# Optimization experiments

Measured on AMD Instinct MI355X. Metric: run time of the kernel, lower is better.

## Reference

```python
import jax, jax.numpy as jnp
import numpy as np

B, H, S, D = 2, 16, 2048, 128  # batch, heads, seq_len, head_dim (hidden=2048, heads=16)


def setup_inputs() -> dict:
    key = jax.random.key(0)
    kq, kk, kv = jax.random.split(key, 3)
    q = jax.random.normal(kq, (B, H, S, D), dtype=jnp.float32)
    k = jax.random.normal(kk, (B, H, S, D), dtype=jnp.float32)
    v = jax.random.normal(kv, (B, H, S, D), dtype=jnp.float32)
    return {"q": q, "k": k, "v": v}


def reference(q, k, v):
    # scores = (q @ k^T) / sqrt(head_dim)  -> [B, H, S, S]
    scaling = 1.0 / jnp.sqrt(jnp.asarray(q.shape[-1], dtype=q.dtype))
    scores = jnp.einsum('bhqd,bhkd->bhqk', q, k) * scaling
    # softmax over keys (dropout p=0.0 -> identity in eval / p=0)
    weights = jax.nn.softmax(scores, axis=-1)
    # out = weights @ v -> [B, H, S, D]
    return jnp.einsum('bhqk,bhkd->bhqd', weights, v)
```

## Files before the change

kernel.cpp:

```cpp
#include <hip/hip_runtime.h>
#include <stdint.h>

typedef __attribute__((ext_vector_type(4))) float f32x4;
typedef __attribute__((ext_vector_type(16))) float f32x16;
typedef __attribute__((ext_vector_type(8))) short bf16x8;

constexpr int S_ = 2048;
constexpr int D_ = 128;
constexpr int BH = 32;
constexpr int KB = 64;
constexpr int NT = S_ / KB;
constexpr float QSCALE = 0.08838834764831845f * 1.4426950408889634f;

__device__ __forceinline__ short f2bf(float f) {
  uint32_t u = __float_as_uint(f);
  u += 0x7fffu + ((u >> 16) & 1u);
  return (short)(u >> 16);
}

__device__ __forceinline__ void gll16(const void* g, void* l) {
  __builtin_amdgcn_global_load_lds(
      (const __attribute__((address_space(1))) void*)g,
      (__attribute__((address_space(3))) void*)l, 16, 0, 0);
}

__global__ void prep_k(const float* __restrict__ k, short* __restrict__ kb) {
  const size_t N8 = (size_t)BH * S_ * D_ / 8;
  size_t i = (size_t)blockIdx.x * blockDim.x + threadIdx.x;
  const size_t stride = (size_t)gridDim.x * blockDim.x;
  for (; i < N8; i += stride) {
    float4 a = reinterpret_cast<const float4*>(k)[i * 2];
    float4 b = reinterpret_cast<const float4*>(k)[i * 2 + 1];
    bf16x8 o;
    o[0] = f2bf(a.x); o[1] = f2bf(a.y); o[2] = f2bf(a.z); o[3] = f2bf(a.w);
    o[4] = f2bf(b.x); o[5] = f2bf(b.y); o[6] = f2bf(b.z); o[7] = f2bf(b.w);
    reinterpret_cast<bf16x8*>(kb)[i] = o;
  }
}

__global__ void prep_vt(const float* __restrict__ v, short* __restrict__ vt) {
  __shared__ __align__(16) short Lt[64][136];
  const int bh = blockIdx.x >> 5;
  const int s0 = (blockIdx.x & 31) * 64;
  const int t = threadIdx.x;
#pragma unroll
  for (int i = 0; i < 4; ++i) {
    int g = t + 256 * i;
    int r = g >> 4, c8 = g & 15;
    const float* src = v + ((size_t)bh * S_ + s0 + r) * D_ + c8 * 8;
    float4 f0 = *reinterpret_cast<const float4*>(src);
    float4 f1 = *reinterpret_cast<const float4*>(src + 4);
    bf16x8 o;
    o[0] = f2bf(f0.x); o[1] = f2bf(f0.y); o[2] = f2bf(f0.z); o[3] = f2bf(f0.w);
    o[4] = f2bf(f1.x); o[5] = f2bf(f1.y); o[6] = f2bf(f1.z); o[7] = f2bf(f1.w);
    *reinterpret_cast<bf16x8*>(&Lt[r][c8 * 8]) = o;
  }
  __syncthreads();
#pragma unroll
  for (int i = 0; i < 4; ++i) {
    int g = t * 4 + i;
    int d = g >> 3, s8 = g & 7;
    bf16x8 o;
#pragma unroll
    for (int j = 0; j < 8; ++j) o[j] = Lt[s8 * 8 + j][d];
    *reinterpret_cast<bf16x8*>(&vt[((size_t)bh * D_ + d) * S_ + s0 + s8 * 8]) = o;
  }
}

__global__ __launch_bounds__(256, 2) void attn_fwd_v4(
    const float* __restrict__ q, const short* __restrict__ kbf,
    const short* __restrict__ vt, float* __restrict__ out)
{
  __shared__ __align__(16) short Klds[2][64 * 128];
  __shared__ __align__(16) short Vlds[2][128 * 64];

  const int lid = blockIdx.x;
  const int swz = (lid & 7) * 64 + (lid >> 3);
  const int qt = swz & 15;
  const int bh = swz >> 4;

  const int tid = threadIdx.x;
  const int wid = tid >> 6;
  const int lane = tid & 63;
  const int l32 = lane & 31;
  const int hi = lane >> 5;

  const int qrow = qt * 128 + wid * 32 + l32;

  bf16x8 bq[8];
  {
    const float* qg = q + ((size_t)bh * S_ + qrow) * D_ + hi * 8;
#pragma unroll
    for (int s = 0; s < 8; ++s) {
      float4 f0 = *reinterpret_cast<const float4*>(qg + s * 16);
      float4 f1 = *reinterpret_cast<const float4*>(qg + s * 16 + 4);
      bf16x8 a;
      a[0] = f2bf(f0.x * QSCALE); a[1] = f2bf(f0.y * QSCALE);
      a[2] = f2bf(f0.z * QSCALE); a[3] = f2bf(f0.w * QSCALE);
      a[4] = f2bf(f1.x * QSCALE); a[5] = f2bf(f1.y * QSCALE);
      a[6] = f2bf(f1.z * QSCALE); a[7] = f2bf(f1.w * QSCALE);
      bq[s] = a;
    }
  }

  const short* kg = kbf + (size_t)bh * S_ * D_;
  const short* vg = vt + (size_t)bh * D_ * S_;

  auto stage = [&](int buf, int kv0) {
#pragma unroll
    for (int j = 0; j < 4; ++j)
      gll16(kg + (size_t)kv0 * D_ + lane * D_ + (j * 4 + wid) * 8,
            &Klds[buf][(j * 256 + wid * 64) * 8]);
#pragma unroll
    for (int j = 0; j < 4; ++j)
      gll16(vg + kv0 + (size_t)((wid & 1) * 64 + lane) * S_ + (j * 2 + (wid >> 1)) * 8,
            &Vlds[buf][(j * 256 + wid * 64) * 8]);
  };

  float m = -1e30f, l = 0.f;
  f32x16 oacc[4];
#pragma unroll
  for (int d0 = 0; d0 < 4; ++d0)
#pragma unroll
    for (int r = 0; r < 16; ++r) oacc[d0][r] = 0.f;

  stage(0, 0);
  int cur = 0;
  for (int t = 0; t < NT; ++t) {
    __syncthreads();
    if (t + 1 < NT) stage(cur ^ 1, (t + 1) * KB);

    const short* Kb = &Klds[cur][0];
    const short* Vb = &Vlds[cur][0];

    f32x16 sf0, sf1;
#pragma unroll
    for (int r = 0; r < 16; ++r) { sf0[r] = 0.f; sf1[r] = 0.f; }
    __builtin_amdgcn_s_setprio(1);
#pragma unroll
    for (int s = 0; s < 8; ++s) {
      bf16x8 k0 = *reinterpret_cast<const bf16x8*>(
          &Kb[((s * 2 + hi) * 64 + l32) * 8]);
      bf16x8 k1 = *reinterpret_cast<const bf16x8*>(
          &Kb[((s * 2 + hi) * 64 + 32 + l32) * 8]);
      sf0 = __builtin_amdgcn_mfma_f32_32x32x16_bf16(k0, bq[s], sf0, 0, 0, 0);
      sf1 = __builtin_amdgcn_mfma_f32_32x32x16_bf16(k1, bq[s], sf1, 0, 0, 0);
    }
    __builtin_amdgcn_s_setprio(0);

    float pm = fmaxf(sf0[0], sf0[1]);
#pragma unroll
    for (int r = 2; r < 16; ++r) pm = fmaxf(pm, sf0[r]);
#pragma unroll
    for (int r = 0; r < 16; ++r) pm = fmaxf(pm, sf1[r]);
    pm = fmaxf(pm, __shfl_xor(pm, 32, 64));
    if (__any(pm > m + 8.f)) {
      const float mo = m;
      m = fmaxf(mo, pm);
      const float al = exp2f(mo - m);
      l *= al;
#pragma unroll
      for (int d0 = 0; d0 < 4; ++d0)
#pragma unroll
        for (int r = 0; r < 16; ++r) oacc[d0][r] *= al;
    }

    float ps = 0.f;
#define PROCESS_CHUNK(SF, C)                                                    \
    {                                                                           \
      uint32_t w[8];                                                            \
      _Pragma("unroll")                                                         \
      for (int i2 = 0; i2 < 8; ++i2) {                                          \
        float e0 = exp2f(SF[2 * i2] - m);                                       \
        float e1 = exp2f(SF[2 * i2 + 1] - m);                                   \
        ps += e0 + e1;                                                          \
        asm("v_cvt_pk_bf16_f32 %0, %1, %2" : "=v"(w[i2]) : "v"(e0), "v"(e1));   \
      }                                                                         \
      asm("v_permlane32_swap_b32 %0, %1" : "+v"(w[0]), "+v"(w[2]));             \
      asm("v_permlane32_swap_b32 %0, %1" : "+v"(w[1]), "+v"(w[3]));             \
      asm("v_permlane32_swap_b32 %0, %1" : "+v"(w[4]), "+v"(w[6]));             \
      asm("v_permlane32_swap_b32 %0, %1" : "+v"(w[5]), "+v"(w[7]));             \
      union { int4 i4; bf16x8 b; } u0, u1;                                      \
      u0.i4 = (int4){(int)w[0], (int)w[1], (int)w[2], (int)w[3]};               \
      u1.i4 = (int4){(int)w[4], (int)w[5], (int)w[6], (int)w[7]};               \
      __builtin_amdgcn_s_setprio(1);                                            \
      _Pragma("unroll")                                                         \
      for (int d0 = 0; d0 < 4; ++d0) {                                          \
        bf16x8 av = *reinterpret_cast<const bf16x8*>(                           \
            &Vb[(((C) * 4 + hi) * 128 + d0 * 32 + l32) * 8]);                   \
        oacc[d0] = __builtin_amdgcn_mfma_f32_32x32x16_bf16(av, u0.b, oacc[d0], 0, 0, 0); \
      }                                                                         \
      _Pragma("unroll")                                                         \
      for (int d0 = 0; d0 < 4; ++d0) {                                          \
        bf16x8 av = *reinterpret_cast<const bf16x8*>(                           \
            &Vb[(((C) * 4 + 2 + hi) * 128 + d0 * 32 + l32) * 8]);               \
        oacc[d0] = __builtin_amdgcn_mfma_f32_32x32x16_bf16(av, u1.b, oacc[d0], 0, 0, 0); \
      }                                                                         \
      __builtin_amdgcn_s_setprio(0);                                            \
    }

    PROCESS_CHUNK(sf0, 0)
    PROCESS_CHUNK(sf1, 1)
#undef PROCESS_CHUNK

    ps += __shfl_xor(ps, 32, 64);
    l += ps;
    cur ^= 1;
  }

  const float inv = 1.0f / l;
  float* ob = out + ((size_t)bh * S_ + qrow) * D_;
#pragma unroll
  for (int d0 = 0; d0 < 4; ++d0)
#pragma unroll
    for (int r2 = 0; r2 < 4; ++r2) {
      float4 o4 = {oacc[d0][r2 * 4 + 0] * inv, oacc[d0][r2 * 4 + 1] * inv,
                   oacc[d0][r2 * 4 + 2] * inv, oacc[d0][r2 * 4 + 3] * inv};
      *reinterpret_cast<float4*>(ob + d0 * 32 + r2 * 8 + hi * 4) = o4;
    }
}

__global__ __launch_bounds__(256, 4) void attn_fwd_v1(
    const float* __restrict__ q, const float* __restrict__ k,
    const float* __restrict__ v, float* __restrict__ out)
{
  __shared__ __align__(16) short Klds[32 * 128];
  __shared__ __align__(16) short Vlds[128 * 40];
  __shared__ __align__(16) short Plds[4][16 * 40];
  const int lid = blockIdx.x;
  const int swz = (lid & 7) * 128 + (lid >> 3);
  const int qt = swz & 31;
  const int bh = swz >> 5;
  const int tid = threadIdx.x;
  const int wid = tid >> 6;
  const int lane = tid & 63;
  const int l16 = lane & 15;
  const int lhi = lane >> 4;
  const int qrow0 = qt * 64 + wid * 16;
  const float* qg = q + ((size_t)bh * S_ + qrow0 + l16) * D_;
  const float* kg = k + (size_t)bh * S_ * D_;
  const float* vg = v + (size_t)bh * S_ * D_;
  bf16x8 aq[4];
#pragma unroll
  for (int ks = 0; ks < 4; ++ks) {
    const float* p = qg + ks * 32 + lhi * 8;
    float4 f0 = *reinterpret_cast<const float4*>(p);
    float4 f1 = *reinterpret_cast<const float4*>(p + 4);
    bf16x8 a;
    a[0] = f2bf(f0.x * QSCALE); a[1] = f2bf(f0.y * QSCALE);
    a[2] = f2bf(f0.z * QSCALE); a[3] = f2bf(f0.w * QSCALE);
    a[4] = f2bf(f1.x * QSCALE); a[5] = f2bf(f1.y * QSCALE);
    a[6] = f2bf(f1.z * QSCALE); a[7] = f2bf(f1.w * QSCALE);
    aq[ks] = a;
  }
  float mrow[4], lrow[4];
  f32x4 oacc[8];
#pragma unroll
  for (int r = 0; r < 4; ++r) { mrow[r] = -1e30f; lrow[r] = 0.f; }
#pragma unroll
  for (int i = 0; i < 8; ++i) oacc[i] = (f32x4){0.f, 0.f, 0.f, 0.f};
  for (int t = 0; t < S_ / 32; ++t) {
    const int kv0 = t * 32;
    __syncthreads();
#pragma unroll
    for (int i = 0; i < 2; ++i) {
      const int g = tid * 2 + i;
      const int row = g >> 4;
      const int c8 = g & 15;
      const float* ksrc = kg + (size_t)(kv0 + row) * D_ + c8 * 8;
      float4 f0 = *reinterpret_cast<const float4*>(ksrc);
      float4 f1 = *reinterpret_cast<const float4*>(ksrc + 4);
      bf16x8 kk;
      kk[0] = f2bf(f0.x); kk[1] = f2bf(f0.y); kk[2] = f2bf(f0.z); kk[3] = f2bf(f0.w);
      kk[4] = f2bf(f1.x); kk[5] = f2bf(f1.y); kk[6] = f2bf(f1.z); kk[7] = f2bf(f1.w);
      *reinterpret_cast<bf16x8*>(
          &Klds[row * D_ + ((c8 * 8) ^ ((row & 7) << 3))]) = kk;
      const float* vsrc = vg + (size_t)(kv0 + row) * D_ + c8 * 8;
      float4 g0 = *reinterpret_cast<const float4*>(vsrc);
      float4 g1 = *reinterpret_cast<const float4*>(vsrc + 4);
      const int dbase = c8 * 8;
      Vlds[(dbase + 0) * 40 + row] = f2bf(g0.x);
      Vlds[(dbase + 1) * 40 + row] = f2bf(g0.y);
      Vlds[(dbase + 2) * 40 + row] = f2bf(g0.z);
      Vlds[(dbase + 3) * 40 + row] = f2bf(g0.w);
      Vlds[(dbase + 4) * 40 + row] = f2bf(g1.x);
      Vlds[(dbase + 5) * 40 + row] = f2bf(g1.y);
      Vlds[(dbase + 6) * 40 + row] = f2bf(g1.z);
      Vlds[(dbase + 7) * 40 + row] = f2bf(g1.w);
    }
    __syncthreads();
    f32x4 sfrag[2];
#pragma unroll
    for (int kb = 0; kb < 2; ++kb) {
      f32x4 acc = (f32x4){0.f, 0.f, 0.f, 0.f};
#pragma unroll
      for (int ks = 0; ks < 4; ++ks) {
        const int rowk = kb * 16 + l16;
        bf16x8 bk = *reinterpret_cast<const bf16x8*>(
            &Klds[rowk * D_ + (((ks * 4 + lhi) * 8) ^ ((rowk & 7) << 3))]);
        acc = __builtin_amdgcn_mfma_f32_16x16x32_bf16(aq[ks], bk, acc, 0, 0, 0);
      }
      sfrag[kb] = acc;
    }
    float mt[4];
#pragma unroll
    for (int r = 0; r < 4; ++r) mt[r] = fmaxf(sfrag[0][r], sfrag[1][r]);
#pragma unroll
    for (int off = 1; off < 16; off <<= 1)
#pragma unroll
      for (int r = 0; r < 4; ++r) mt[r] = fmaxf(mt[r], __shfl_xor(mt[r], off, 64));
    float al[4], ps[4];
#pragma unroll
    for (int r = 0; r < 4; ++r) {
      float mn = fmaxf(mrow[r], mt[r]);
      al[r] = exp2f(mrow[r] - mn);
      mrow[r] = mn;
      ps[r] = 0.f;
    }
#pragma unroll
    for (int kb = 0; kb < 2; ++kb)
#pragma unroll
      for (int r = 0; r < 4; ++r) {
        float p = exp2f(sfrag[kb][r] - mrow[r]);
        ps[r] += p;
        Plds[wid][(lhi * 4 + r) * 40 + kb * 16 + l16] = f2bf(p);
      }
#pragma unroll
    for (int off = 1; off < 16; off <<= 1)
#pragma unroll
      for (int r = 0; r < 4; ++r) ps[r] += __shfl_xor(ps[r], off, 64);
#pragma unroll
    for (int r = 0; r < 4; ++r) lrow[r] = lrow[r] * al[r] + ps[r];
#pragma unroll
    for (int i = 0; i < 8; ++i)
#pragma unroll
      for (int r = 0; r < 4; ++r) oacc[i][r] *= al[r];
    bf16x8 ap = *reinterpret_cast<const bf16x8*>(&Plds[wid][l16 * 40 + lhi * 8]);
#pragma unroll
    for (int d0 = 0; d0 < 8; ++d0) {
      bf16x8 bv = *reinterpret_cast<const bf16x8*>(
          &Vlds[(d0 * 16 + l16) * 40 + lhi * 8]);
      oacc[d0] = __builtin_amdgcn_mfma_f32_16x16x32_bf16(ap, bv, oacc[d0], 0, 0, 0);
    }
  }
#pragma unroll
  for (int r = 0; r < 4; ++r) {
    float inv = 1.0f / lrow[r];
    float* orow = out + ((size_t)bh * S_ + qrow0 + lhi * 4 + r) * D_ + l16;
#pragma unroll
    for (int d0 = 0; d0 < 8; ++d0) orow[d0 * 16] = oacc[d0][r] * inv;
  }
}

extern "C" void kernel_launch(void* const* d_in, const int* in_sizes, int n_in,
                              void* d_out, int out_size, void* d_ws, size_t ws_size,
                              hipStream_t stream) {
  (void)in_sizes; (void)n_in; (void)out_size;
  const float* q = (const float*)d_in[0];
  const float* k = (const float*)d_in[1];
  const float* v = (const float*)d_in[2];
  float* o = (float*)d_out;
  const size_t NEL = (size_t)BH * S_ * D_;
  const size_t need = NEL * 2 * sizeof(short);
  if (ws_size >= need) {
    short* kb = (short*)d_ws;
    short* vt = kb + NEL;
    hipLaunchKernelGGL(prep_k, dim3(2048), dim3(256), 0, stream, k, kb);
    hipLaunchKernelGGL(prep_vt, dim3(1024), dim3(256), 0, stream, v, vt);
    hipLaunchKernelGGL(attn_fwd_v4, dim3(512), dim3(256), 0, stream, q, kb, vt, o);
  } else {
    hipLaunchKernelGGL(attn_fwd_v1, dim3(1024), dim3(256), 0, stream, q, k, v, o);
  }
}
```

Measured before the change: 126.2 us.

## Switch attention kernel to 16x16x32 MFMA with 64-row query tiles and 32-key blocks

Rewrites the main attention kernel to use 16x16x32 bf16 MFMA instead of 32x32x16. Each block now covers 64 query rows and each step 32 keys, and the launch doubles to 1024 blocks with occupancy raised to 4 blocks per CU. The aim is to shrink per-block LDS and register use and fill the machine with more resident waves. In exchange, K/V tiles from LDS are reused across fewer query rows and there are twice as many loop iterations, each with its own barrier and softmax rescale overhead.

```diff
diff --git a/kernel.cpp b/kernel.cpp
--- a/kernel.cpp
+++ b/kernel.cpp
@@ -2,13 +2,12 @@
 #include <stdint.h>
 
 typedef __attribute__((ext_vector_type(4))) float f32x4;
-typedef __attribute__((ext_vector_type(16))) float f32x16;
 typedef __attribute__((ext_vector_type(8))) short bf16x8;
 
 constexpr int S_ = 2048;
 constexpr int D_ = 128;
 constexpr int BH = 32;
-constexpr int KB = 64;
+constexpr int KB = 32;
 constexpr int NT = S_ / KB;
 constexpr float QSCALE = 0.08838834764831845f * 1.4426950408889634f;
 
@@ -67,62 +66,68 @@
   }
 }
 
-__global__ __launch_bounds__(256, 2) void attn_fwd_v4(
+__global__ __launch_bounds__(256, 4) void attn_fwd_v5(
     const float* __restrict__ q, const short* __restrict__ kbf,
     const short* __restrict__ vt, float* __restrict__ out)
 {
-  __shared__ __align__(16) short Klds[2][64 * 128];
-  __shared__ __align__(16) short Vlds[2][128 * 64];
+  __shared__ __align__(16) short Klds[2][KB * D_];
+  __shared__ __align__(16) short Vlds[2][D_ * KB];
 
   const int lid = blockIdx.x;
-  const int swz = (lid & 7) * 64 + (lid >> 3);
-  const int qt = swz & 15;
-  const int bh = swz >> 4;
+  const int swz = (lid & 7) * 128 + (lid >> 3);
+  const int qt = swz & 31;
+  const int bh = swz >> 5;
 
   const int tid = threadIdx.x;
   const int wid = tid >> 6;
   const int lane = tid & 63;
-  const int l32 = lane & 31;
-  const int hi = lane >> 5;
-
-  const int qrow = qt * 128 + wid * 32 + l32;
-
-  bf16x8 bq[8];
+  const int l16 = lane & 15;
+  const int lhi = lane >> 4;
+
+  const int qrow = qt * 64 + wid * 16 + l16;
+
+  bf16x8 bq[4];
   {
-    const float* qg = q + ((size_t)bh * S_ + qrow) * D_ + hi * 8;
-#pragma unroll
-    for (int s = 0; s < 8; ++s) {
-      float4 f0 = *reinterpret_cast<const float4*>(qg + s * 16);
-      float4 f1 = *reinterpret_cast<const float4*>(qg + s * 16 + 4);
+    const float* qg = q + ((size_t)bh * S_ + qrow) * D_ + lhi * 8;
+#pragma unroll
+    for (int ks = 0; ks < 4; ++ks) {
+      float4 f0 = *reinterpret_cast<const float4*>(qg + ks * 32);
+      float4 f1 = *reinterpret_cast<const float4*>(qg + ks * 32 + 4);
       bf16x8 a;
       a[0] = f2bf(f0.x * QSCALE); a[1] = f2bf(f0.y * QSCALE);
       a[2] = f2bf(f0.z * QSCALE); a[3] = f2bf(f0.w * QSCALE);
       a[4] = f2bf(f1.x * QSCALE); a[5] = f2bf(f1.y * QSCALE);
       a[6] = f2bf(f1.z * QSCALE); a[7] = f2bf(f1.w * QSCALE);
-      bq[s] = a;
+      bq[ks] = a;
     }
   }
 
   const short* kg = kbf + (size_t)bh * S_ * D_;
   const short* vg = vt + (size_t)bh * D_ * S_;
 
+  int koff[2], voff[2];
+#pragma unroll
+  for (int j = 0; j < 2; ++j) {
+    const int G = tid + 256 * j;
+    koff[j] = (G & 31) * D_ + (G >> 5) * 8;
+    voff[j] = (G & 127) * S_ + (G >> 7) * 8;
+  }
+
   auto stage = [&](int buf, int kv0) {
 #pragma unroll
-    for (int j = 0; j < 4; ++j)
-      gll16(kg + (size_t)kv0 * D_ + lane * D_ + (j * 4 + wid) * 8,
+    for (int j = 0; j < 2; ++j)
+      gll16(kg + (size_t)kv0 * D_ + koff[j],
             &Klds[buf][(j * 256 + wid * 64) * 8]);
 #pragma unroll
-    for (int j = 0; j < 4; ++j)
-      gll16(vg + kv0 + (size_t)((wid & 1) * 64 + lane) * S_ + (j * 2 + (wid >> 1)) * 8,
+    for (int j = 0; j < 2; ++j)
+      gll16(vg + kv0 + voff[j],
             &Vlds[buf][(j * 256 + wid * 64) * 8]);
   };
 
   float m = -1e30f, l = 0.f;
-  f32x16 oacc[4];
-#pragma unroll
-  for (int d0 = 0; d0 < 4; ++d0)
-#pragma unroll
-    for (int r = 0; r < 16; ++r) oacc[d0][r] = 0.f;
+  f32x4 oacc[8];
+#pragma unroll
+  for (int dd = 0; dd < 8; ++dd) oacc[dd] = (f32x4){0.f, 0.f, 0.f, 0.f};
 
   stage(0, 0);
   int cur = 0;
@@ -133,26 +138,22 @@
     const short* Kb = &Klds[cur][0];
     const short* Vb = &Vlds[cur][0];
 
-    f32x16 sf0, sf1;
-#pragma unroll
-    for (int r = 0; r < 16; ++r) { sf0[r] = 0.f; sf1[r] = 0.f; }
+    f32x4 sf0 = (f32x4){0.f, 0.f, 0.f, 0.f};
+    f32x4 sf1 = (f32x4){0.f, 0.f, 0.f, 0.f};
     __builtin_amdgcn_s_setprio(1);
 #pragma unroll
-    for (int s = 0; s < 8; ++s) {
-      bf16x8 k0 = *reinterpret_cast<const bf16x8*>(
-          &Kb[((s * 2 + hi) * 64 + l32) * 8]);
-      bf16x8 k1 = *reinterpret_cast<const bf16x8*>(
-          &Kb[((s * 2 + hi) * 64 + 32 + l32) * 8]);
-      sf0 = __builtin_amdgcn_mfma_f32_32x32x16_bf16(k0, bq[s], sf0, 0, 0, 0);
-      sf1 = __builtin_amdgcn_mfma_f32_32x32x16_bf16(k1, bq[s], sf1, 0, 0, 0);
+    for (int ks = 0; ks < 4; ++ks) {
+      const int g = (ks * 4 + lhi) * 32;
+      bf16x8 a0 = *reinterpret_cast<const bf16x8*>(&Kb[(g + l16) * 8]);
+      bf16x8 a1 = *reinterpret_cast<const bf16x8*>(&Kb[(g + 16 + l16) * 8]);
+      sf0 = __builtin_amdgcn_mfma_f32_16x16x32_bf16(a0, bq[ks], sf0, 0, 0, 0);
+      sf1 = __builtin_amdgcn_mfma_f32_16x16x32_bf16(a1, bq[ks], sf1, 0, 0, 0);
     }
     __builtin_amdgcn_s_setprio(0);
 
-    float pm = fmaxf(sf0[0], sf0[1]);
-#pragma unroll
-    for (int r = 2; r < 16; ++r) pm = fmaxf(pm, sf0[r]);
-#pragma unroll
-    for (int r = 0; r < 16; ++r) pm = fmaxf(pm, sf1[r]);
+    float pm = fmaxf(fmaxf(fmaxf(sf0[0], sf0[1]), fmaxf(sf0[2], sf0[3])),
+                     fmaxf(fmaxf(sf1[0], sf1[1]), fmaxf(sf1[2], sf1[3])));
+    pm = fmaxf(pm, __shfl_xor(pm, 16, 64));
     pm = fmaxf(pm, __shfl_xor(pm, 32, 64));
     if (__any(pm > m + 8.f)) {
       const float mo = m;
@@ -160,64 +161,50 @@
       const float al = exp2f(mo - m);
       l *= al;
 #pragma unroll
-      for (int d0 = 0; d0 < 4; ++d0)
-#pragma unroll
-        for (int r = 0; r < 16; ++r) oacc[d0][r] *= al;
-    }
-
-    float ps = 0.f;
-#define PROCESS_CHUNK(SF, C)                                                    \
-    {                                                                           \
-      uint32_t w[8];                                                            \
-      _Pragma("unroll")                                                         \
-      for (int i2 = 0; i2 < 8; ++i2) {                                          \
-        float e0 = exp2f(SF[2 * i2] - m);                                       \
-        float e1 = exp2f(SF[2 * i2 + 1] - m);                                   \
-        ps += e0 + e1;                                                          \
-        asm("v_cvt_pk_bf16_f32 %0, %1, %2" : "=v"(w[i2]) : "v"(e0), "v"(e1));   \
-      }                                                                         \
-      asm("v_permlane32_swap_b32 %0, %1" : "+v"(w[0]), "+v"(w[2]));             \
-      asm("v_permlane32_swap_b32 %0, %1" : "+v"(w[1]), "+v"(w[3]));             \
-      asm("v_permlane32_swap_b32 %0, %1" : "+v"(w[4]), "+v"(w[6]));             \
-      asm("v_permlane32_swap_b32 %0, %1" : "+v"(w[5]), "+v"(w[7]));             \
-      union { int4 i4; bf16x8 b; } u0, u1;                                      \
-      u0.i4 = (int4){(int)w[0], (int)w[1], (int)w[2], (int)w[3]};               \
-      u1.i4 = (int4){(int)w[4], (int)w[5], (int)w[6], (int)w[7]};               \
-      __builtin_amdgcn_s_setprio(1);                                            \
-      _Pragma("unroll")                                                         \
-      for (int d0 = 0; d0 < 4; ++d0) {                                          \
-        bf16x8 av = *reinterpret_cast<const bf16x8*>(                           \
-            &Vb[(((C) * 4 + hi) * 128 + d0 * 32 + l32) * 8]);                   \
-        oacc[d0] = __builtin_amdgcn_mfma_f32_32x32x16_bf16(av, u0.b, oacc[d0], 0, 0, 0); \
-      }                                                                         \
-      _Pragma("unroll")                                                         \
-      for (int d0 = 0; d0 < 4; ++d0) {                                          \
-        bf16x8 av = *reinterpret_cast<const bf16x8*>(                           \
-            &Vb[(((C) * 4 + 2 + hi) * 128 + d0 * 32 + l32) * 8]);               \
-        oacc[d0] = __builtin_amdgcn_mfma_f32_32x32x16_bf16(av, u1.b, oacc[d0], 0, 0, 0); \
-      }                                                                         \
-      __builtin_amdgcn_s_setprio(0);                                            \
-    }
-
-    PROCESS_CHUNK(sf0, 0)
-    PROCESS_CHUNK(sf1, 1)
-#undef PROCESS_CHUNK
-
+      for (int dd = 0; dd < 8; ++dd) oacc[dd] *= al;
+    }
+
+    float e00 = exp2f(sf0[0] - m), e01 = exp2f(sf0[1] - m);
+    float e02 = exp2f(sf0[2] - m), e03 = exp2f(sf0[3] - m);
+    float e10 = exp2f(sf1[0] - m), e11 = exp2f(sf1[1] - m);
+    float e12 = exp2f(sf1[2] - m), e13 = exp2f(sf1[3] - m);
+    float ps = ((e00 + e01) + (e02 + e03)) + ((e10 + e11) + (e12 + e13));
+
+    uint32_t x0, x1, y0, y1;
+    asm("v_cvt_pk_bf16_f32 %0, %1, %2" : "=v"(x0) : "v"(e00), "v"(e01));
+    asm("v_cvt_pk_bf16_f32 %0, %1, %2" : "=v"(x1) : "v"(e02), "v"(e03));
+    asm("v_cvt_pk_bf16_f32 %0, %1, %2" : "=v"(y0) : "v"(e10), "v"(e11));
+    asm("v_cvt_pk_bf16_f32 %0, %1, %2" : "=v"(y1) : "v"(e12), "v"(e13));
+    asm("v_permlane32_swap_b32 %0, %1" : "+v"(x0), "+v"(y0));
+    asm("v_permlane32_swap_b32 %0, %1" : "+v"(x1), "+v"(y1));
+    asm("v_permlane16_swap_b32 %0, %1" : "+v"(x0), "+v"(y0));
+    asm("v_permlane16_swap_b32 %0, %1" : "+v"(x1), "+v"(y1));
+    union { int4 i4; bf16x8 b; } pb;
+    pb.i4 = (int4){(int)x0, (int)x1, (int)y0, (int)y1};
+
+    ps += __shfl_xor(ps, 16, 64);
     ps += __shfl_xor(ps, 32, 64);
     l += ps;
+
+    __builtin_amdgcn_s_setprio(1);
+#pragma unroll
+    for (int dd = 0; dd < 8; ++dd) {
+      bf16x8 av = *reinterpret_cast<const bf16x8*>(
+          &Vb[(lhi * 128 + dd * 16 + l16) * 8]);
+      oacc[dd] = __builtin_amdgcn_mfma_f32_16x16x32_bf16(av, pb.b, oacc[dd], 0, 0, 0);
+    }
+    __builtin_amdgcn_s_setprio(0);
     cur ^= 1;
   }
 
   const float inv = 1.0f / l;
   float* ob = out + ((size_t)bh * S_ + qrow) * D_;
 #pragma unroll
-  for (int d0 = 0; d0 < 4; ++d0)
-#pragma unroll
-    for (int r2 = 0; r2 < 4; ++r2) {
-      float4 o4 = {oacc[d0][r2 * 4 + 0] * inv, oacc[d0][r2 * 4 + 1] * inv,
-                   oacc[d0][r2 * 4 + 2] * inv, oacc[d0][r2 * 4 + 3] * inv};
-      *reinterpret_cast<float4*>(ob + d0 * 32 + r2 * 8 + hi * 4) = o4;
-    }
+  for (int dd = 0; dd < 8; ++dd) {
+    float4 o4 = {oacc[dd][0] * inv, oacc[dd][1] * inv,
+                 oacc[dd][2] * inv, oacc[dd][3] * inv};
+    *reinterpret_cast<float4*>(ob + dd * 16 + lhi * 4) = o4;
+  }
 }
 
 __global__ __launch_bounds__(256, 4) void attn_fwd_v1(
@@ -367,7 +354,7 @@
     short* vt = kb + NEL;
     hipLaunchKernelGGL(prep_k, dim3(2048), dim3(256), 0, stream, k, kb);
     hipLaunchKernelGGL(prep_vt, dim3(1024), dim3(256), 0, stream, v, vt);
-    hipLaunchKernelGGL(attn_fwd_v4, dim3(512), dim3(256), 0, stream, q, kb, vt, o);
+    hipLaunchKernelGGL(attn_fwd_v5, dim3(1024), dim3(256), 0, stream, q, kb, vt, o);
   } else {
     hipLaunchKernelGGL(attn_fwd_v1, dim3(1024), dim3(256), 0, stream, q, k, v, o);
   }
```

Measured after the change: 153.1 us. +21.4%, slower.
